# Kernel tuning notes

Measured on AMD Instinct MI355X. Metric: run time of the kernel, lower is better.

Reference implementation:

```python
import jax, jax.numpy as jnp
import numpy as np

B, C, NS, NT, H = 8, 256, 16384, 8192, 8
D = C // H  # 32
EPS_ATTN = 1e-6
EPS_LN = 1e-5


def _layernorm(x, g, b):
    m = jnp.mean(x, axis=-1, keepdims=True)
    v = jnp.mean((x - m) ** 2, axis=-1, keepdims=True)
    return (x - m) * jax.lax.rsqrt(v + EPS_LN) * g + b


def setup_inputs() -> dict:
    key = jax.random.key(0)
    ks = jax.random.split(key, 16)
    s = lambda fan_in: 1.0 / np.sqrt(fan_in)
    return {
        "search_feat": jax.random.normal(ks[0], (B, C, NS), jnp.float32),
        "search_xyz": jax.random.normal(ks[1], (B, NS, 3), jnp.float32),
        "template_feat": jax.random.normal(ks[2], (B, C, NT), jnp.float32),
        "template_xyz": jax.random.normal(ks[3], (B, NT, 3), jnp.float32),
        # pos_mlp: Linear(3, C) -> ReLU -> Linear(C, C); weights stored [in, out]
        "pos_w1": jax.random.uniform(ks[4], (3, C), jnp.float32, -s(3), s(3)),
        "pos_b1": jnp.zeros((C,), jnp.float32),
        "pos_w2": jax.random.uniform(ks[5], (C, C), jnp.float32, -s(C), s(C)),
        "pos_b2": jnp.zeros((C,), jnp.float32),
        "q_w": jax.random.uniform(ks[6], (C, C), jnp.float32, -s(C), s(C)),
        "k_w": jax.random.uniform(ks[7], (C, C), jnp.float32, -s(C), s(C)),
        "v_w": jax.random.uniform(ks[8], (C, C), jnp.float32, -s(C), s(C)),
        "merge_w": jax.random.uniform(ks[9], (C, C), jnp.float32, -s(C), s(C)),
        "mlp_w1": jax.random.uniform(ks[10], (2 * C, 2 * C), jnp.float32, -s(2 * C), s(2 * C)),
        "mlp_w2": jax.random.uniform(ks[11], (2 * C, C), jnp.float32, -s(2 * C), s(2 * C)),
        "ln1_g": jnp.ones((C,), jnp.float32),
        "ln1_b": jnp.zeros((C,), jnp.float32),
        "ln2_g": jnp.ones((C,), jnp.float32),
        "ln2_b": jnp.zeros((C,), jnp.float32),
    }


def _forward(search_feat, search_xyz, template_feat, template_xyz,
             pos_w1, pos_b1, pos_w2, pos_b2, q_w, k_w, v_w, merge_w,
             mlp_w1, mlp_w2, ln1_g, ln1_b, ln2_g, ln2_b):
    bs = search_feat.shape[0]
    sf = jnp.transpose(search_feat, (0, 2, 1))     # [B, Ns, C]
    tf = jnp.transpose(template_feat, (0, 2, 1))   # [B, Nt, C]
    # positional encoding added to template features before value projection
    pos = jax.nn.relu(template_xyz @ pos_w1 + pos_b1) @ pos_w2 + pos_b2
    tfp = tf + pos
    q = (sf @ q_w).reshape(bs, -1, H, D)    # [B, Ns, H, D]
    k = (tf @ k_w).reshape(bs, -1, H, D)    # [B, Nt, H, D]
    v = (tfp @ v_w).reshape(bs, -1, H, D)   # [B, Nt, H, D]
    # linear attention with elu+1 feature map
    Q = jax.nn.elu(q) + 1.0
    K = jax.nn.elu(k) + 1.0
    v_len = v.shape[1]
    v_scaled = v / v_len
    KV = jnp.einsum('nshd,nshv->nhdv', K, v_scaled)            # [B, H, D, D]
    Z = 1.0 / (jnp.einsum('nlhd,nhd->nlh', Q, K.sum(axis=1)) + EPS_ATTN)
    msg = jnp.einsum('nlhd,nhdv,nlh->nlhv', Q, KV, Z) * v_len  # [B, Ns, H, D]
    msg = msg.reshape(bs, -1, H * D) @ merge_w
    msg = _layernorm(msg, ln1_g, ln1_b)
    msg = jax.nn.relu(jnp.concatenate([sf, msg], axis=2) @ mlp_w1) @ mlp_w2
    msg = _layernorm(msg, ln2_g, ln2_b)
    return jnp.transpose(sf + msg, (0, 2, 1))  # [B, C, Ns]


def reference(search_feat, search_xyz, template_feat, template_xyz,
              pos_w1, pos_b1, pos_w2, pos_b2, q_w, k_w, v_w, merge_w,
              mlp_w1, mlp_w2, ln1_g, ln1_b, ln2_g, ln2_b):
    return _forward(search_feat, search_xyz, template_feat, template_xyz,
                    pos_w1, pos_b1, pos_w2, pos_b2, q_w, k_w, v_w, merge_w,
                    mlp_w1, mlp_w2, ln1_g, ln1_b, ln2_g, ln2_b)
```

## Files before the change

### kernel.cpp

```cpp
#include <hip/hip_runtime.h>
#include <math.h>

#define B_  8
#define C_  256
#define NS_ 16384
#define NT_ 8192
#define H_  8
#define D_  32
#define C2_ 512
#define NCH 4
#define KVZ_ (H_*D_*D_ + H_*D_)

typedef __attribute__((ext_vector_type(8))) short bf16x8;
typedef __attribute__((ext_vector_type(4))) short bf16x4;
typedef __attribute__((ext_vector_type(4))) float f32x4;

__device__ __forceinline__ short f2bf(float f) {
    unsigned u = __float_as_uint(f);
    u = (u + 0x7fffu + ((u >> 16) & 1u)) >> 16;
    return (short)u;
}
__device__ __forceinline__ float bf2f(short s) {
    return __uint_as_float(((unsigned)(unsigned short)s) << 16);
}
__device__ __forceinline__ float2 bfpair(unsigned u) {
    float2 r;
    r.x = __uint_as_float(u << 16);
    r.y = __uint_as_float(u & 0xffff0000u);
    return r;
}
__device__ __forceinline__ void load_lds16(const void* g, void* l) {
    __builtin_amdgcn_global_load_lds(
        (const __attribute__((address_space(1))) unsigned int*)g,
        (__attribute__((address_space(3))) unsigned int*)l, 16, 0, 0);
}

__global__ __launch_bounds__(256)
void castT(const float* __restrict__ in, short* __restrict__ ob, int NLEN, int b0)
{
    __shared__ float tl[32][33];
    int g = blockIdx.z, gb = b0 + g;
    int n0 = blockIdx.x * 32, c0 = blockIdx.y * 32;
    int t = threadIdx.x, tr = t >> 5, tc = t & 31;
    #pragma unroll
    for (int i = 0; i < 4; ++i)
        tl[tr + 8*i][tc] = in[((size_t)gb*C_ + c0 + tr + 8*i)*NLEN + n0 + tc];
    __syncthreads();
    #pragma unroll
    for (int i = 0; i < 4; ++i)
        ob[((size_t)g*NLEN + n0 + tr + 8*i)*C_ + c0 + tc] = f2bf(tl[tc][tr + 8*i]);
}

struct WDesc { const float* src; int K; int N; int off; };
struct WPack { WDesc d[7]; };

__global__ __launch_bounds__(256)
void wcast_all(WPack p, short* __restrict__ wt)
{
    __shared__ float tl[32][33];
    WDesc d = p.d[blockIdx.z];
    int kt = blockIdx.x * 32, nt = blockIdx.y * 32;
    if (kt >= d.K || nt >= d.N) return;
    int t = threadIdx.x, tr = t >> 5, tc = t & 31;
    #pragma unroll
    for (int i = 0; i < 4; ++i)
        tl[tr + 8*i][tc] = d.src[(size_t)(kt + tr + 8*i)*d.N + nt + tc];
    __syncthreads();
    short* o = wt + d.off;
    #pragma unroll
    for (int i = 0; i < 4; ++i)
        o[(size_t)(nt + tr + 8*i)*d.K + kt + tc] = f2bf(tl[tc][tr + 8*i]);
}

__global__ __launch_bounds__(256)
void pos_h(const float* __restrict__ xyz, const float* __restrict__ w1,
           const float* __restrict__ b1, short* __restrict__ hb, int b0)
{
    int g = blockIdx.y, gb = b0 + g;
    int r0 = blockIdx.x * 16;
    int t = threadIdx.x;
    float w1x = w1[t], w1y = w1[C_ + t], w1z = w1[2*C_ + t], bb = b1[t];
    for (int r = 0; r < 16; ++r) {
        const float* p = xyz + ((size_t)gb*NT_ + r0 + r)*3;
        float h = fmaxf(p[0]*w1x + p[1]*w1y + p[2]*w1z + bb, 0.f);
        hb[((size_t)g*NT_ + r0 + r)*C_ + t] = f2bf(h);
    }
}

template<int EPI, int NF>
__global__ __launch_bounds__(256)
void gemm_bf16(const short* __restrict__ A0, int lda0,
               const short* __restrict__ A1, int lda1, int split,
               const short* __restrict__ Wt,
               const float* __restrict__ bias,
               const short* __restrict__ addmat,
               short* __restrict__ outp,
               int M, int N, int K)
{
    __shared__ __align__(16) short As[128*32];
    __shared__ __align__(16) short Bs[NF*32*32];
    int g = blockIdx.z;
    int nb = blockIdx.x * (NF*32);
    int mb = blockIdx.y * 128;
    int t = threadIdx.x;
    int lane = t & 63;
    int w = t >> 6, wr = w >> 1, wc = w & 1;

    const short* A0g = A0 + (size_t)g*M*lda0;
    const short* A1g = A1 ? (A1 + (size_t)g*M*lda1) : A0;

    f32x4 acc[4][NF] = {};

    int r4 = t >> 2;
    int ch = t & 3;

    for (int kb = 0; kb < K; kb += 32) {
        const short* Ab; int lda, kc;
        if (kb < split) { Ab = A0g; lda = lda0; kc = kb; }
        else            { Ab = A1g; lda = lda1; kc = kb - split; }
        const short* as0 = Ab + (size_t)(mb + r4)*lda + kc + ch*8;
        load_lds16(as0,                   &As[r4*32 + ch*8]);
        load_lds16(as0 + (size_t)64*lda,  &As[(r4 + 64)*32 + ch*8]);
        #pragma unroll
        for (int i = 0; i < NF/2; ++i) {
            int row = r4 + 64*i;
            load_lds16(Wt + (size_t)(nb + row)*K + kb + ch*8, &Bs[row*32 + ch*8]);
        }
        __syncthreads();

        int kq = (lane >> 4) * 8;
        bf16x8 af[4], bfr[NF];
        #pragma unroll
        for (int m = 0; m < 4; ++m)
            af[m] = *(const bf16x8*)&As[(wr*64 + m*16 + (lane & 15))*32 + kq];
        #pragma unroll
        for (int n = 0; n < NF; ++n)
            bfr[n] = *(const bf16x8*)&Bs[(wc*(NF*16) + n*16 + (lane & 15))*32 + kq];
        #pragma unroll
        for (int m = 0; m < 4; ++m)
            #pragma unroll
            for (int n = 0; n < NF; ++n)
                acc[m][n] = __builtin_amdgcn_mfma_f32_16x16x32_bf16(
                    af[m], bfr[n], acc[m][n], 0, 0, 0);
        __syncthreads();
    }

    short* og = outp + (size_t)g*M*N;
    const short* am = (EPI == 3) ? (addmat + (size_t)g*M*N) : nullptr;
    int rq = (lane >> 4) * 4;
    int cl = lane & 15;
    #pragma unroll
    for (int m = 0; m < 4; ++m) {
        #pragma unroll
        for (int r = 0; r < 4; ++r) {
            int row = mb + wr*64 + m*16 + rq + r;
            size_t ro = (size_t)row * N;
            #pragma unroll
            for (int n = 0; n < NF; ++n) {
                int col = nb + wc*(NF*16) + n*16 + cl;
                float v = acc[m][n][r];
                if constexpr (EPI == 1) v = fmaxf(v, 0.f);
                if constexpr (EPI == 2) v = (v > 0.f) ? (v + 1.f) : __expf(v);
                if constexpr (EPI == 3) v = v + bias[col] + bf2f(am[ro + col]);
                og[ro + col] = f2bf(v);
            }
        }
    }
}

__global__ __launch_bounds__(256)
void kv_kernel(const short* __restrict__ Kb, const short* __restrict__ Vb,
               float* __restrict__ kvz)
{
    __shared__ float SK[32][D_];
    __shared__ float SV[32][D_];
    int h = blockIdx.x, chk = blockIdx.y, g = blockIdx.z;
    int t = threadIdx.x;
    int d = t >> 3, v0 = (t & 7) * 4;
    int lr = t >> 3, lc = (t & 7) * 4;
    float acc[4] = {0.f, 0.f, 0.f, 0.f};
    float ksum = 0.f;
    int s0beg = chk * (NT_/NCH), s0end = s0beg + NT_/NCH;
    for (int s0 = s0beg; s0 < s0end; s0 += 32) {
        size_t off = ((size_t)g*NT_ + s0 + lr)*C_ + h*D_ + lc;
        uint2 ku = *(const uint2*)(Kb + off);
        uint2 vu = *(const uint2*)(Vb + off);
        float2 k0 = bfpair(ku.x), k1 = bfpair(ku.y);
        float2 w0 = bfpair(vu.x), w1 = bfpair(vu.y);
        SK[lr][lc] = k0.x; SK[lr][lc+1] = k0.y; SK[lr][lc+2] = k1.x; SK[lr][lc+3] = k1.y;
        SV[lr][lc] = w0.x; SV[lr][lc+1] = w0.y; SV[lr][lc+2] = w1.x; SV[lr][lc+3] = w1.y;
        __syncthreads();
        #pragma unroll
        for (int ss = 0; ss < 32; ++ss) {
            float kd = SK[ss][d];
            #pragma unroll
            for (int j = 0; j < 4; ++j) acc[j] += kd * SV[ss][v0 + j];
            ksum += kd;
        }
        __syncthreads();
    }
    float* KV = kvz + ((size_t)g*NCH + chk)*KVZ_;
    #pragma unroll
    for (int j = 0; j < 4; ++j) KV[h*D_*D_ + d*D_ + v0 + j] = acc[j];
    if ((t & 7) == 0) KV[H_*D_*D_ + h*D_ + d] = ksum;
}

__global__ __launch_bounds__(256)
void kvfin(const float* __restrict__ kvp, short* __restrict__ KVT,
           float* __restrict__ KSf)
{
    int g = blockIdx.x, t = threadIdx.x;
    const float* p = kvp + (size_t)g*NCH*KVZ_;
    for (int idx = t; idx < H_*D_*D_; idx += 256) {
        int h = idx >> 10, rem = idx & 1023, v = rem >> 5, d = rem & 31;
        float s = 0.f;
        #pragma unroll
        for (int c = 0; c < NCH; ++c) s += p[c*KVZ_ + h*1024 + d*32 + v];
        KVT[(size_t)g*8192 + h*1024 + v*32 + d] = f2bf(s);
    }
    {
        float s = 0.f;
        #pragma unroll
        for (int c = 0; c < NCH; ++c) s += p[c*KVZ_ + H_*D_*D_ + t];
        KSf[(size_t)g*256 + t] = s;
    }
}

__global__ __launch_bounds__(256)
void qam_kernel(const short* __restrict__ sfb, const short* __restrict__ wtq,
                const short* __restrict__ wtm, const short* __restrict__ KVT,
                const float* __restrict__ KSf,
                const float* __restrict__ ln1g, const float* __restrict__ ln1b,
                short* __restrict__ mrg)
{
    __shared__ short QT[64][264];
    __shared__ __align__(16) short As[64*32];
    __shared__ __align__(16) short Bs[256*32];
    __shared__ float sredS[4][64], sredQ[4][64];
    __shared__ float mrM[64], mrR[64];
    __shared__ float gbet[512];

    int g = blockIdx.y;
    int l0 = blockIdx.x * 64;
    int t = threadIdx.x;
    int lane = t & 63, w = t >> 6;
    int lx = lane & 15, ly = lane >> 4;

    gbet[t]       = ln1g[t];
    gbet[256 + t] = ln1b[t];

    const short* sfg = sfb + ((size_t)g*NS_ + l0)*C_;

    f32x4 acc[4][4] = {};
    for (int kb = 0; kb < C_; kb += 32) {
        load_lds16(sfg + (size_t)(t>>2)*C_ + kb + (t&3)*8, &As[(t>>2)*32 + (t&3)*8]);
        #pragma unroll
        for (int i = 0; i < 4; ++i) {
            int row = (t>>2) + 64*i;
            load_lds16(wtq + (size_t)row*C_ + kb + (t&3)*8, &Bs[row*32 + (t&3)*8]);
        }
        __syncthreads();
        bf16x8 af[4], bfv[4];
        #pragma unroll
        for (int m = 0; m < 4; ++m)
            af[m] = *(const bf16x8*)&Bs[(w*64 + m*16 + lx)*32 + ly*8];
        #pragma unroll
        for (int n = 0; n < 4; ++n)
            bfv[n] = *(const bf16x8*)&As[(n*16 + lx)*32 + ly*8];
        #pragma unroll
        for (int m = 0; m < 4; ++m)
            #pragma unroll
            for (int n = 0; n < 4; ++n)
                acc[m][n] = __builtin_amdgcn_mfma_f32_16x16x32_bf16(
                    af[m], bfv[n], acc[m][n], 0, 0, 0);
        __syncthreads();
    }
    #pragma unroll
    for (int m = 0; m < 4; ++m) {
        int c0 = w*64 + m*16 + ly*4;
        #pragma unroll
        for (int n = 0; n < 4; ++n) {
            bf16x4 pk;
            #pragma unroll
            for (int r = 0; r < 4; ++r) {
                float v = acc[m][n][r];
                pk[r] = f2bf((v > 0.f) ? (v + 1.f) : __expf(v));
            }
            *(bf16x4*)&QT[n*16 + lx][c0] = pk;
        }
    }
    __syncthreads();

    const short* kvg = KVT + (size_t)g*8192;
    bf16x8 bq[2][4];
    #pragma unroll
    for (int hh = 0; hh < 2; ++hh)
        #pragma unroll
        for (int n = 0; n < 4; ++n)
            bq[hh][n] = *(const bf16x8*)&QT[n*16 + lx][(2*w + hh)*32 + ly*8];
    float z[2][4];
    #pragma unroll
    for (int hh = 0; hh < 2; ++hh) {
        const float* kp = KSf + (size_t)g*256 + (2*w + hh)*32 + ly*8;
        float4 ka = *(const float4*)kp;
        float4 kb4 = *(const float4*)(kp + 4);
        float kr[8] = {ka.x, ka.y, ka.z, ka.w, kb4.x, kb4.y, kb4.z, kb4.w};
        #pragma unroll
        for (int n = 0; n < 4; ++n) {
            float s = 0.f;
            #pragma unroll
            for (int j = 0; j < 8; ++j) s += bf2f(bq[hh][n][j]) * kr[j];
            s += __shfl_xor(s, 16);
            s += __shfl_xor(s, 32);
            z[hh][n] = 1.f / (s + 1e-6f);
        }
    }
    f32x4 zero = {0.f, 0.f, 0.f, 0.f};
    f32x4 a2[4][4];
    #pragma unroll
    for (int m = 0; m < 4; ++m) {
        int h = 2*w + (m >> 1);
        bf16x8 afk = *(const bf16x8*)(kvg + ((size_t)h*1024 + ((m&1)*16 + lx)*32 + ly*8));
        #pragma unroll
        for (int n = 0; n < 4; ++n)
            a2[m][n] = __builtin_amdgcn_mfma_f32_16x16x32_bf16(
                afk, bq[m>>1][n], zero, 0, 0, 0);
    }
    #pragma unroll
    for (int m = 0; m < 4; ++m) {
        int c0 = w*64 + m*16 + ly*4;
        #pragma unroll
        for (int n = 0; n < 4; ++n) {
            bf16x4 pk;
            #pragma unroll
            for (int r = 0; r < 4; ++r)
                pk[r] = f2bf(a2[m][n][r] * z[m>>1][n]);
            *(bf16x4*)&QT[n*16 + lx][c0] = pk;
        }
    }
    __syncthreads();

    f32x4 acc3[4][4] = {};
    for (int kb = 0; kb < C_; kb += 32) {
        #pragma unroll
        for (int i = 0; i < 4; ++i) {
            int row = (t>>2) + 64*i;
            load_lds16(wtm + (size_t)row*C_ + kb + (t&3)*8, &Bs[row*32 + (t&3)*8]);
        }
        __syncthreads();
        bf16x8 af[4], bfv[4];
        #pragma unroll
        for (int m = 0; m < 4; ++m)
            af[m] = *(const bf16x8*)&Bs[(w*64 + m*16 + lx)*32 + ly*8];
        #pragma unroll
        for (int n = 0; n < 4; ++n)
            bfv[n] = *(const bf16x8*)&QT[n*16 + lx][kb + ly*8];
        #pragma unroll
        for (int m = 0; m < 4; ++m)
            #pragma unroll
            for (int n = 0; n < 4; ++n)
                acc3[m][n] = __builtin_amdgcn_mfma_f32_16x16x32_bf16(
                    af[m], bfv[n], acc3[m][n], 0, 0, 0);
        __syncthreads();
    }

    float sP[4] = {0,0,0,0}, qP[4] = {0,0,0,0};
    #pragma unroll
    for (int n = 0; n < 4; ++n)
        #pragma unroll
        for (int m = 0; m < 4; ++m)
            #pragma unroll
            for (int r = 0; r < 4; ++r) {
                float v = acc3[m][n][r];
                sP[n] += v; qP[n] += v*v;
            }
    #pragma unroll
    for (int n = 0; n < 4; ++n) {
        sP[n] += __shfl_xor(sP[n], 16); sP[n] += __shfl_xor(sP[n], 32);
        qP[n] += __shfl_xor(qP[n], 16); qP[n] += __shfl_xor(qP[n], 32);
    }
    if (ly == 0) {
        #pragma unroll
        for (int n = 0; n < 4; ++n) {
            sredS[w][n*16 + lx] = sP[n];
            sredQ[w][n*16 + lx] = qP[n];
        }
    }
    __syncthreads();
    if (t < 64) {
        float s = 0.f, q = 0.f;
        #pragma unroll
        for (int ww = 0; ww < 4; ++ww) { s += sredS[ww][t]; q += sredQ[ww][t]; }
        float m = s * (1.f/C_);
        mrM[t] = m;
        mrR[t] = rsqrtf(q*(1.f/C_) - m*m + 1e-5f);
    }
    __syncthreads();
    #pragma unroll
    for (int n = 0; n < 4; ++n) {
        float mn = mrM[n*16 + lx], rs = mrR[n*16 + lx];
        #pragma unroll
        for (int m = 0; m < 4; ++m) {
            int c0 = w*64 + m*16 + ly*4;
            bf16x4 pk;
            #pragma unroll
            for (int r = 0; r < 4; ++r) {
                int c = c0 + r;
                pk[r] = f2bf((acc3[m][n][r] - mn)*rs*gbet[c] + gbet[256 + c]);
            }
            *(bf16x4*)&QT[n*16 + lx][c0] = pk;
        }
    }
    __syncthreads();
    short* og = mrg + ((size_t)g*NS_ + l0)*C_;
    int row = t >> 2;
    #pragma unroll
    for (int i = 0; i < 8; ++i) {
        int chk = (t & 3) + 4*i;
        *(uint4*)(og + (size_t)row*C_ + chk*8) = *(const uint4*)&QT[row][chk*8];
    }
}

__global__ __launch_bounds__(256)
void m2f_kernel(const short* __restrict__ hid, const short* __restrict__ wt2,
                const float* __restrict__ sfeat,
                const float* __restrict__ ln2g, const float* __restrict__ ln2b,
                float* __restrict__ out, int b0)
{
    __shared__ __align__(16) short As[256*32];
    __shared__ __align__(16) short Bs[64*32];
    __shared__ float sredS[4][64], sredQ[4][64];
    __shared__ float mrM[64], mrR[64];
    __shared__ float gbet[512];

    int g = blockIdx.y, gb = b0 + g;
    int l0 = blockIdx.x * 64;
    int t = threadIdx.x;
    int lane = t & 63, w = t >> 6;
    int lx = lane & 15, ly = lane >> 4;

    gbet[t]       = ln2g[t];
    gbet[256 + t] = ln2b[t];

    const short* hg = hid + ((size_t)g*NS_ + l0)*C2_;
    f32x4 acc[4][4] = {};
    for (int kb = 0; kb < C2_; kb += 32) {
        #pragma unroll
        for (int i = 0; i < 4; ++i) {
            int row = (t>>2) + 64*i;
            load_lds16(wt2 + (size_t)row*C2_ + kb + (t&3)*8, &As[row*32 + (t&3)*8]);
        }
        load_lds16(hg + (size_t)(t>>2)*C2_ + kb + (t&3)*8, &Bs[(t>>2)*32 + (t&3)*8]);
        __syncthreads();
        bf16x8 af[4], bfv[4];
        #pragma unroll
        for (int m = 0; m < 4; ++m)
            af[m] = *(const bf16x8*)&As[(w*64 + m*16 + lx)*32 + ly*8];
        #pragma unroll
        for (int n = 0; n < 4; ++n)
            bfv[n] = *(const bf16x8*)&Bs[(n*16 + lx)*32 + ly*8];
        #pragma unroll
        for (int m = 0; m < 4; ++m)
            #pragma unroll
            for (int n = 0; n < 4; ++n)
                acc[m][n] = __builtin_amdgcn_mfma_f32_16x16x32_bf16(
                    af[m], bfv[n], acc[m][n], 0, 0, 0);
        __syncthreads();
    }

    float sP[4] = {0,0,0,0}, qP[4] = {0,0,0,0};
    #pragma unroll
    for (int n = 0; n < 4; ++n)
        #pragma unroll
        for (int m = 0; m < 4; ++m)
            #pragma unroll
            for (int r = 0; r < 4; ++r) {
                float v = acc[m][n][r];
                sP[n] += v; qP[n] += v*v;
            }
    #pragma unroll
    for (int n = 0; n < 4; ++n) {
        sP[n] += __shfl_xor(sP[n], 16); sP[n] += __shfl_xor(sP[n], 32);
        qP[n] += __shfl_xor(qP[n], 16); qP[n] += __shfl_xor(qP[n], 32);
    }
    if (ly == 0) {
        #pragma unroll
        for (int n = 0; n < 4; ++n) {
            sredS[w][n*16 + lx] = sP[n];
            sredQ[w][n*16 + lx] = qP[n];
        }
    }
    __syncthreads();
    if (t < 64) {
        float s = 0.f, q = 0.f;
        #pragma unroll
        for (int ww = 0; ww < 4; ++ww) { s += sredS[ww][t]; q += sredQ[ww][t]; }
        float m = s * (1.f/C_);
        mrM[t] = m;
        mrR[t] = rsqrtf(q*(1.f/C_) - m*m + 1e-5f);
    }
    __syncthreads();

    #pragma unroll
    for (int n = 0; n < 4; ++n) {
        int l = n*16 + lx;
        float mn = mrM[l], rs = mrR[l];
        #pragma unroll
        for (int m = 0; m < 4; ++m) {
            #pragma unroll
            for (int r = 0; r < 4; ++r) {
                int c = w*64 + m*16 + ly*4 + r;
                size_t o = ((size_t)gb*C_ + c)*NS_ + l0 + l;
                out[o] = sfeat[o] + (acc[m][n][r] - mn)*rs*gbet[c] + gbet[256 + c];
            }
        }
    }
}

extern "C" void kernel_launch(void* const* d_in, const int* in_sizes, int n_in,
                              void* d_out, int out_size, void* d_ws, size_t ws_size,
                              hipStream_t stream)
{
    (void)in_sizes; (void)n_in; (void)out_size;
    const float* search_feat   = (const float*)d_in[0];
    const float* template_feat = (const float*)d_in[2];
    const float* template_xyz  = (const float*)d_in[3];
    const float* pos_w1  = (const float*)d_in[4];
    const float* pos_b1  = (const float*)d_in[5];
    const float* pos_w2  = (const float*)d_in[6];
    const float* pos_b2  = (const float*)d_in[7];
    const float* q_w     = (const float*)d_in[8];
    const float* k_w     = (const float*)d_in[9];
    const float* v_w     = (const float*)d_in[10];
    const float* merge_w = (const float*)d_in[11];
    const float* mlp_w1  = (const float*)d_in[12];
    const float* mlp_w2  = (const float*)d_in[13];
    const float* ln1_g   = (const float*)d_in[14];
    const float* ln1_b   = (const float*)d_in[15];
    const float* ln2_g   = (const float*)d_in[16];
    const float* ln2_b   = (const float*)d_in[17];
    float* out = (float*)d_out;

    const int W_Q = 0, W_K = 65536, W_V = 131072, W_M = 196608,
              W_P = 262144, W_1 = 327680, W_2 = 589824;
    const size_t wElems = 720896;

    size_t sfE = (size_t)NS_*C_, tfE = (size_t)NT_*C_;
    int G = 8;
    while (G > 1) {
        size_t shorts = (size_t)G*(4*sfE + 2*tfE) + wElems + (size_t)G*8192;
        size_t bytes  = shorts*2 + (size_t)G*NCH*KVZ_*4 + (size_t)G*256*4 + 512;
        if (bytes <= ws_size) break;
        G >>= 1;
    }

    short* wtb  = (short*)d_ws;
    short* sfb  = wtb  + wElems;
    short* tfb  = sfb  + (size_t)G*sfE;
    short* tfpb = tfb  + (size_t)G*tfE;
    short* hid  = tfpb + (size_t)G*tfE;
    short* mrgb = hid  + (size_t)2*G*sfE;
    short* KVTb = mrgb + (size_t)G*sfE;
    float* kvpf = (float*)(KVTb + (size_t)G*8192);
    float* KSfb = kvpf + (size_t)G*NCH*KVZ_;
    short* Kb = hid;
    short* Vb = hid + (size_t)G*tfE;
    short* hb = hid + (size_t)2*G*tfE;

    WPack pack;
    pack.d[0] = { q_w,     C_,  C_,  W_Q };
    pack.d[1] = { k_w,     C_,  C_,  W_K };
    pack.d[2] = { v_w,     C_,  C_,  W_V };
    pack.d[3] = { merge_w, C_,  C_,  W_M };
    pack.d[4] = { pos_w2,  C_,  C_,  W_P };
    pack.d[5] = { mlp_w1,  C2_, C2_, W_1 };
    pack.d[6] = { mlp_w2,  C2_, C_,  W_2 };
    wcast_all<<<dim3(16, 16, 7), 256, 0, stream>>>(pack, wtb);

    for (int b0 = 0; b0 < B_; b0 += G) {
        castT<<<dim3(NS_/32, C_/32, G), 256, 0, stream>>>(search_feat, sfb, NS_, b0);
        castT<<<dim3(NT_/32, C_/32, G), 256, 0, stream>>>(template_feat, tfb, NT_, b0);
        pos_h<<<dim3(NT_/16, G), 256, 0, stream>>>(template_xyz, pos_w1, pos_b1, hb, b0);
        gemm_bf16<3,4><<<dim3(C_/128, NT_/128, G), 256, 0, stream>>>(
            hb, C_, nullptr, 0, 1<<30, wtb + W_P, pos_b2, tfb, tfpb, NT_, C_, C_);
        gemm_bf16<2,4><<<dim3(C_/128, NT_/128, G), 256, 0, stream>>>(
            tfb, C_, nullptr, 0, 1<<30, wtb + W_K, nullptr, nullptr, Kb, NT_, C_, C_);
        gemm_bf16<0,4><<<dim3(C_/128, NT_/128, G), 256, 0, stream>>>(
            tfpb, C_, nullptr, 0, 1<<30, wtb + W_V, nullptr, nullptr, Vb, NT_, C_, C_);
        kv_kernel<<<dim3(H_, NCH, G), 256, 0, stream>>>(Kb, Vb, kvpf);
        kvfin<<<dim3(G), 256, 0, stream>>>(kvpf, KVTb, KSfb);
        qam_kernel<<<dim3(NS_/64, G), 256, 0, stream>>>(
            sfb, wtb + W_Q, wtb + W_M, KVTb, KSfb, ln1_g, ln1_b, mrgb);
        gemm_bf16<1,4><<<dim3(C2_/128, NS_/128, G), 256, 0, stream>>>(
            sfb, C_, mrgb, C_, C_, wtb + W_1, nullptr, nullptr, hid, NS_, C2_, C2_);
        m2f_kernel<<<dim3(NS_/64, G), 256, 0, stream>>>(
            hid, wtb + W_2, search_feat, ln2_g, ln2_b, out, b0);
    }
}
```

Measured before the change: 601.5 us.

## Fold pos_mlp second layer into value projection and coalesce final output writes

Result: faster. 537.8 us (-10.6%).

```diff
diff --git a/kernel.cpp b/kernel.cpp
--- a/kernel.cpp
+++ b/kernel.cpp
@@ -51,7 +51,7 @@
         ob[((size_t)g*NLEN + n0 + tr + 8*i)*C_ + c0 + tc] = f2bf(tl[tc][tr + 8*i]);
 }
 
-struct WDesc { const float* src; int K; int N; int off; };
+struct WDesc { const float* src; int K; int N; int off; int ldo; };
 struct WPack { WDesc d[7]; };
 
 __global__ __launch_bounds__(256)
@@ -69,7 +69,29 @@
     short* o = wt + d.off;
     #pragma unroll
     for (int i = 0; i < 4; ++i)
-        o[(size_t)(nt + tr + 8*i)*d.K + kt + tc] = f2bf(tl[tc][tr + 8*i]);
+        o[(size_t)(nt + tr + 8*i)*d.ldo + kt + tc] = f2bf(tl[tc][tr + 8*i]);
+}
+
+__global__ __launch_bounds__(256)
+void fusew(short* __restrict__ wv2, const short* __restrict__ wp,
+           const float* __restrict__ b2, const float* __restrict__ v_w,
+           float* __restrict__ bv)
+{
+    int n = blockIdx.x, k = threadIdx.x;
+    __shared__ float vrow[256];
+    __shared__ float bred[256];
+    vrow[k] = bf2f(wv2[(size_t)n*512 + k]);
+    bred[k] = b2[k] * v_w[(size_t)k*C_ + n];
+    __syncthreads();
+    float s = 0.f;
+    for (int m = 0; m < 256; ++m)
+        s += vrow[m] * bf2f(wp[m*256 + k]);
+    wv2[(size_t)n*512 + 256 + k] = f2bf(s);
+    for (int off2 = 128; off2 > 0; off2 >>= 1) {
+        __syncthreads();
+        if (k < off2) bred[k] += bred[k + off2];
+    }
+    if (k == 0) bv[n] = bred[0];
 }
 
 __global__ __launch_bounds__(256)
@@ -100,8 +122,17 @@
     __shared__ __align__(16) short As[128*32];
     __shared__ __align__(16) short Bs[NF*32*32];
     int g = blockIdx.z;
-    int nb = blockIdx.x * (NF*32);
-    int mb = blockIdx.y * 128;
+    int nbs = gridDim.x, Mb = gridDim.y;
+    int nb, mb;
+    if ((Mb & 7) == 0) {
+        int lin = blockIdx.y * nbs + blockIdx.x;
+        int xcd = lin & 7, j = lin >> 3;
+        nb = (j % nbs) * (NF*32);
+        mb = ((j / nbs) * 8 + xcd) * 128;
+    } else {
+        nb = blockIdx.x * (NF*32);
+        mb = blockIdx.y * 128;
+    }
     int t = threadIdx.x;
     int lane = t & 63;
     int w = t >> 6, wr = w >> 1, wc = w & 1;
@@ -162,6 +193,7 @@
                 if constexpr (EPI == 1) v = fmaxf(v, 0.f);
                 if constexpr (EPI == 2) v = (v > 0.f) ? (v + 1.f) : __expf(v);
                 if constexpr (EPI == 3) v = v + bias[col] + bf2f(am[ro + col]);
+                if constexpr (EPI == 4) v = v + bias[col];
                 og[ro + col] = f2bf(v);
             }
         }
@@ -421,14 +453,13 @@
     }
 }
 
-__global__ __launch_bounds__(256)
+__global__ __launch_bounds__(256, 4)
 void m2f_kernel(const short* __restrict__ hid, const short* __restrict__ wt2,
                 const float* __restrict__ sfeat,
                 const float* __restrict__ ln2g, const float* __restrict__ ln2b,
                 float* __restrict__ out, int b0)
 {
-    __shared__ __align__(16) short As[256*32];
-    __shared__ __align__(16) short Bs[64*32];
+    __shared__ __align__(16) short sh[64*258];
     __shared__ float sredS[4][64], sredQ[4][64];
     __shared__ float mrM[64], mrR[64];
     __shared__ float gbet[512];
@@ -442,6 +473,9 @@
     gbet[t]       = ln2g[t];
     gbet[256 + t] = ln2b[t];
 
+    short* As = sh;
+    short* Bs = sh + 8192;
+
     const short* hg = hid + ((size_t)g*NS_ + l0)*C2_;
     f32x4 acc[4][4] = {};
     for (int kb = 0; kb < C2_; kb += 32) {
@@ -507,13 +541,22 @@
         float mn = mrM[l], rs = mrR[l];
         #pragma unroll
         for (int m = 0; m < 4; ++m) {
-            #pragma unroll
-            for (int r = 0; r < 4; ++r) {
-                int c = w*64 + m*16 + ly*4 + r;
-                size_t o = ((size_t)gb*C_ + c)*NS_ + l0 + l;
-                out[o] = sfeat[o] + (acc[m][n][r] - mn)*rs*gbet[c] + gbet[256 + c];
-            }
-        }
+            int c0 = w*64 + m*16 + ly*4;
+            #pragma unroll
+            for (int r = 0; r < 4; ++r)
+                sh[l*258 + c0 + r] =
+                    f2bf((acc[m][n][r] - mn)*rs*gbet[c0+r] + gbet[256 + c0 + r]);
+        }
+    }
+    __syncthreads();
+
+    int l = t & 63, cg = t >> 6;
+    const float* sfp = sfeat + (size_t)gb*C_*NS_ + l0;
+    float* op = out + (size_t)gb*C_*NS_ + l0;
+    for (int ci = 0; ci < 64; ++ci) {
+        int c = cg*64 + ci;
+        size_t o = (size_t)c*NS_ + l;
+        op[o] = sfp[o] + bf2f(sh[l*258 + c]);
     }
 }
 
@@ -541,15 +584,15 @@
     const float* ln2_b   = (const float*)d_in[17];
     float* out = (float*)d_out;
 
-    const int W_Q = 0, W_K = 65536, W_V = 131072, W_M = 196608,
-              W_P = 262144, W_1 = 327680, W_2 = 589824;
-    const size_t wElems = 720896;
+    const int W_Q = 0, W_K = 65536, W_M = 131072, W_P = 196608,
+              W_1 = 262144, W_2 = 524288, W_V2 = 655360;
+    const size_t wElems = 786432;
 
     size_t sfE = (size_t)NS_*C_, tfE = (size_t)NT_*C_;
     int G = 8;
     while (G > 1) {
-        size_t shorts = (size_t)G*(4*sfE + 2*tfE) + wElems + (size_t)G*8192;
-        size_t bytes  = shorts*2 + (size_t)G*NCH*KVZ_*4 + (size_t)G*256*4 + 512;
+        size_t shorts = (size_t)G*(4*sfE + tfE + 8192) + wElems;
+        size_t bytes  = shorts*2 + (size_t)G*(NCH*KVZ_ + 256)*4 + 256*4 + 1024;
         if (bytes <= ws_size) break;
         G >>= 1;
     }
@@ -557,36 +600,35 @@
     short* wtb  = (short*)d_ws;
     short* sfb  = wtb  + wElems;
     short* tfb  = sfb  + (size_t)G*sfE;
-    short* tfpb = tfb  + (size_t)G*tfE;
-    short* hid  = tfpb + (size_t)G*tfE;
+    short* hid  = tfb  + (size_t)G*tfE;
     short* mrgb = hid  + (size_t)2*G*sfE;
     short* KVTb = mrgb + (size_t)G*sfE;
     float* kvpf = (float*)(KVTb + (size_t)G*8192);
     float* KSfb = kvpf + (size_t)G*NCH*KVZ_;
+    float* bvf  = KSfb + (size_t)G*256;
     short* Kb = hid;
     short* Vb = hid + (size_t)G*tfE;
     short* hb = hid + (size_t)2*G*tfE;
 
     WPack pack;
-    pack.d[0] = { q_w,     C_,  C_,  W_Q };
-    pack.d[1] = { k_w,     C_,  C_,  W_K };
-    pack.d[2] = { v_w,     C_,  C_,  W_V };
-    pack.d[3] = { merge_w, C_,  C_,  W_M };
-    pack.d[4] = { pos_w2,  C_,  C_,  W_P };
-    pack.d[5] = { mlp_w1,  C2_, C2_, W_1 };
-    pack.d[6] = { mlp_w2,  C2_, C_,  W_2 };
+    pack.d[0] = { q_w,     C_,  C_,  W_Q,  C_  };
+    pack.d[1] = { k_w,     C_,  C_,  W_K,  C_  };
+    pack.d[2] = { merge_w, C_,  C_,  W_M,  C_  };
+    pack.d[3] = { pos_w2,  C_,  C_,  W_P,  C_  };
+    pack.d[4] = { mlp_w1,  C2_, C2_, W_1,  C2_ };
+    pack.d[5] = { mlp_w2,  C2_, C_,  W_2,  C2_ };
+    pack.d[6] = { v_w,     C_,  C_,  W_V2, C2_ };
     wcast_all<<<dim3(16, 16, 7), 256, 0, stream>>>(pack, wtb);
+    fusew<<<dim3(256), 256, 0, stream>>>(wtb + W_V2, wtb + W_P, pos_b2, v_w, bvf);
 
     for (int b0 = 0; b0 < B_; b0 += G) {
         castT<<<dim3(NS_/32, C_/32, G), 256, 0, stream>>>(search_feat, sfb, NS_, b0);
         castT<<<dim3(NT_/32, C_/32, G), 256, 0, stream>>>(template_feat, tfb, NT_, b0);
         pos_h<<<dim3(NT_/16, G), 256, 0, stream>>>(template_xyz, pos_w1, pos_b1, hb, b0);
-        gemm_bf16<3,4><<<dim3(C_/128, NT_/128, G), 256, 0, stream>>>(
-            hb, C_, nullptr, 0, 1<<30, wtb + W_P, pos_b2, tfb, tfpb, NT_, C_, C_);
         gemm_bf16<2,4><<<dim3(C_/128, NT_/128, G), 256, 0, stream>>>(
             tfb, C_, nullptr, 0, 1<<30, wtb + W_K, nullptr, nullptr, Kb, NT_, C_, C_);
-        gemm_bf16<0,4><<<dim3(C_/128, NT_/128, G), 256, 0, stream>>>(
-            tfpb, C_, nullptr, 0, 1<<30, wtb + W_V, nullptr, nullptr, Vb, NT_, C_, C_);
+        gemm_bf16<4,4><<<dim3(C_/128, NT_/128, G), 256, 0, stream>>>(
+            tfb, C_, hb, C_, C_, wtb + W_V2, bvf, nullptr, Vb, NT_, C_, C2_);
         kv_kernel<<<dim3(H_, NCH, G), 256, 0, stream>>>(Kb, Vb, kvpf);
         kvfin<<<dim3(G), 256, 0, stream>>>(kvpf, KVTb, KSfb);
         qam_kernel<<<dim3(NS_/64, G), 256, 0, stream>>>(
```
